# Performance work log

Measured on AMD Instinct MI355X. Metric: run time of the kernel, lower is better.

## Reference

```python
import jax, jax.numpy as jnp
import numpy as np

DIM = 256
NUM_HEADS = 4
WINDOW = 64
EPS = 1e-6


def setup_inputs() -> dict:
    key = jax.random.key(0)
    ks = jax.random.split(key, 12)
    d = DIM
    s = 0.02
    return {
        "x": jax.random.normal(ks[0], (4, 2049, d), dtype=jnp.float32),
        "norm1_w": jnp.ones((d,), jnp.float32),
        "in_proj_w": jax.random.normal(ks[1], (3 * d, d), jnp.float32) * s,
        "in_proj_b": jnp.zeros((3 * d,), jnp.float32),
        "out_proj_w": jax.random.normal(ks[2], (d, d), jnp.float32) * s,
        "out_proj_b": jnp.zeros((d,), jnp.float32),
        "norm2_w": jnp.ones((d,), jnp.float32),
        "w1": jax.random.normal(ks[3], (2 * d, d), jnp.float32) * s,
        "b1": jnp.zeros((2 * d,), jnp.float32),
        "w2": jax.random.normal(ks[4], (d, 2 * d), jnp.float32) * s,
        "b2": jnp.zeros((d,), jnp.float32),
    }


def _rmsnorm(x, w):
    r = jax.lax.rsqrt(jnp.mean(x * x, axis=-1, keepdims=True) + EPS)
    return x * r * w


def _factorized_mask(size):
    # global token 0 attends/attended everywhere; others banded within WINDOW
    idx = jnp.arange(size)
    band = jnp.abs(idx[:, None] - idx[None, :]) <= WINDOW
    allowed = band | (idx[:, None] == 0) | (idx[None, :] == 0)
    return jnp.where(allowed, 0.0, -jnp.inf).astype(jnp.float32)


def reference(x, norm1_w, in_proj_w, in_proj_b, out_proj_w, out_proj_b,
              norm2_w, w1, b1, w2, b2):
    B, S, D = x.shape
    H = NUM_HEADS
    dh = D // H
    residual = x
    h = _rmsnorm(x, norm1_w)
    # fused qkv projection (torch MHA in_proj): [B,S,3D]
    qkv = h @ in_proj_w.T + in_proj_b
    q, k, v = jnp.split(qkv, 3, axis=-1)
    q = q.reshape(B, S, H, dh).transpose(0, 2, 1, 3)  # [B,H,S,dh]
    k = k.reshape(B, S, H, dh).transpose(0, 2, 1, 3)
    v = v.reshape(B, S, H, dh).transpose(0, 2, 1, 3)
    scores = jnp.einsum("bhqd,bhkd->bhqk", q, k) / jnp.sqrt(jnp.float32(dh))
    scores = scores + _factorized_mask(S)  # additive -inf mask
    attn = jax.nn.softmax(scores, axis=-1)
    ctx = jnp.einsum("bhqk,bhkd->bhqd", attn, v)
    ctx = ctx.transpose(0, 2, 1, 3).reshape(B, S, D)
    attn_out = ctx @ out_proj_w.T + out_proj_b
    x1 = residual + attn_out
    h2 = _rmsnorm(x1, norm2_w)
    ffn = jax.nn.gelu(h2 @ w1.T + b1, approximate=False) @ w2.T + b2
    return x1 + ffn
```

## Files before the change

### kernel.cpp

```cpp
#include <hip/hip_runtime.h>
#include <hip/hip_bf16.h>
#include <math.h>

#define BATCH 4
#define SEQ 2049
#define WIN 64
#define M_ROWS 8196
#define M_PAD 8320

#define QT16 129
#define NKB 10
#define PSTR 168
#define CSTR 264
#define VGUARD 64
#define VW 2256
#define QKSTR 512
#define NSPLIT 33
#define VT_F4 288768
#define KCS 520

typedef __attribute__((ext_vector_type(8))) short short8;
typedef __attribute__((ext_vector_type(4))) float f32x4;
typedef __hip_bfloat16 bf16;

__device__ __forceinline__ float b2f(short u) {
    union { unsigned int i; float f; } c;
    c.i = ((unsigned int)(unsigned short)u) << 16;
    return c.f;
}
__device__ __forceinline__ short f2b(float f) {
    bf16 h = __float2bfloat16(f);
    return *reinterpret_cast<short*>(&h);
}

__global__ __launch_bounds__(256) void prep_kernel(
        const float* __restrict__ wq, const float* __restrict__ wo,
        const float* __restrict__ w1, const float* __restrict__ w2,
        bf16* __restrict__ oq, bf16* __restrict__ oo,
        bf16* __restrict__ o1, bf16* __restrict__ o2,
        short* __restrict__ vT) {
    const int bi = blockIdx.x, tid = threadIdx.x;
    if (bi < 2048) {
        int i = bi * 256 + tid;
        if (i < 196608)      oq[i]          = __float2bfloat16(wq[i]);
        else if (i < 262144) oo[i - 196608] = __float2bfloat16(wo[i - 196608]);
        else if (i < 393216) o1[i - 262144] = __float2bfloat16(w1[i - 262144]);
        else                 o2[i - 393216] = __float2bfloat16(w2[i - 393216]);
        return;
    }
    int rowid = (bi - 2048) * 2 + (tid >> 7);
    short* vr = vT + (size_t)rowid * VW;
    int t = tid & 127;
    if (t < 64) vr[t] = 0;
    else {
        int u = t - 64;
        if (u < 143) vr[VGUARD + SEQ + u] = 0;
        if (u + 143 < 143) {}
    }
}

__global__ __launch_bounds__(256) void gemm_qkv(
        const float* __restrict__ x, const float* __restrict__ n1w,
        const bf16* __restrict__ B, const float* __restrict__ bias,
        bf16* __restrict__ qk, short* __restrict__ vT) {
    __shared__ __align__(16) short hA[32 * KCS];
    __shared__ __align__(16) short lB[8 * 128 * 8];
    const int tid = threadIdx.x, lane = tid & 63, wid = tid >> 6;
    const int m0 = blockIdx.x * 64;
    const int n0 = blockIdx.y * 128;
    const int wr = wid >> 1, wc = wid & 1;
    const int r = lane & 15, g = lane >> 4;

    {
        const float4 wv = reinterpret_cast<const float4*>(n1w)[lane];
        #pragma unroll
        for (int t = 0; t < 16; t++) {
            int rr = wid * 16 + t;
            int row = m0 + rr;
            int rowc = row < M_ROWS ? row : M_ROWS - 1;
            const float4 v = reinterpret_cast<const float4*>(x + (size_t)rowc * 256)[lane];
            float ss = v.x * v.x + v.y * v.y + v.z * v.z + v.w * v.w;
            #pragma unroll
            for (int o = 1; o < 64; o <<= 1) ss += __shfl_xor(ss, o, 64);
            float rs = rsqrtf(ss * (1.0f / 256.0f) + 1e-6f);
            short4 y;
            y.x = f2b(v.x * rs * wv.x);
            y.y = f2b(v.y * rs * wv.y);
            y.z = f2b(v.z * rs * wv.z);
            y.w = f2b(v.w * rs * wv.w);
            *reinterpret_cast<short4*>(&hA[(lane >> 1) * KCS + rr * 8 + (lane & 1) * 4]) = y;
        }
    }
    __syncthreads();

    f32x4 acc[2][4];
    #pragma unroll
    for (int i = 0; i < 2; i++)
        #pragma unroll
        for (int j = 0; j < 4; j++) acc[i][j] = (f32x4){0.f, 0.f, 0.f, 0.f};

    for (int k0 = 0; k0 < 256; k0 += 64) {
        const int kcb = k0 >> 3;
        #pragma unroll
        for (int it = 0; it < 4; ++it) {
            int c = it * 256 + tid;
            int kc = c >> 7, row = c & 127;
            __builtin_amdgcn_global_load_lds(
                (const __attribute__((address_space(1))) void*)(B + (size_t)(n0 + row) * 256 + k0 + kc * 8),
                (__attribute__((address_space(3))) void*)&lB[c * 8], 16, 0, 0);
        }
        __syncthreads();
        #pragma unroll
        for (int kk = 0; kk < 2; kk++) {
            short8 a[2], b[4];
            #pragma unroll
            for (int mi = 0; mi < 2; mi++)
                a[mi] = *reinterpret_cast<const short8*>(
                    &hA[(kcb + kk * 4 + g) * KCS + (wr * 32 + mi * 16 + r) * 8]);
            #pragma unroll
            for (int ni = 0; ni < 4; ni++)
                b[ni] = *reinterpret_cast<const short8*>(&lB[((kk * 4 + g) * 128 + wc * 64 + ni * 16 + r) * 8]);
            #pragma unroll
            for (int mi = 0; mi < 2; mi++)
                #pragma unroll
                for (int ni = 0; ni < 4; ni++)
                    acc[mi][ni] = __builtin_amdgcn_mfma_f32_16x16x32_bf16(a[mi], b[ni], acc[mi][ni], 0, 0, 0);
        }
        __syncthreads();
    }

    const int c0 = lane & 15, r0 = (lane >> 4) * 4;
    const bool isV = (n0 >= 512);
    #pragma unroll
    for (int mi = 0; mi < 2; mi++) {
        #pragma unroll
        for (int ni = 0; ni < 4; ni++) {
            int col = n0 + wc * 64 + ni * 16 + c0;
            float bv = bias[col];
            #pragma unroll
            for (int j = 0; j < 4; j++) {
                int row = m0 + wr * 32 + mi * 16 + r0 + j;
                if (row < M_ROWS) {
                    float v = acc[mi][ni][j] + bv;
                    if (!isV) {
                        qk[(size_t)row * QKSTR + col] = __float2bfloat16(v);
                    } else {
                        int dcol = col - 512, hh = dcol >> 6, d = dcol & 63;
                        int bb = row >> 11;
                        int js = row - bb * SEQ;
                        if (js < 0) { bb--; js += SEQ; }
                        vT[((size_t)((bb * 4 + hh) * 64 + d)) * VW + VGUARD + js] = f2b(v);
                    }
                }
            }
        }
    }
}

template<int MODE, int BM, int BN>
__global__ __launch_bounds__(256) void gemm_lds_k(
        const bf16* __restrict__ A, const bf16* __restrict__ B,
        const float* __restrict__ bias, const float* __restrict__ resid,
        void* __restrict__ C, int M, int N, int K) {
    constexpr int FM = BM / 32, FN = BN / 32;
    __shared__ __align__(16) short lA[8 * BM * 8];
    __shared__ __align__(16) short lB[8 * BN * 8];
    const int tid = threadIdx.x, lane = tid & 63, wid = tid >> 6;
    const int m0 = blockIdx.x * BM;
    const int n0 = blockIdx.y * BN;
    const int wr = wid >> 1, wc = wid & 1;
    const int r = lane & 15, g = lane >> 4;

    f32x4 acc[FM][FN];
    #pragma unroll
    for (int i = 0; i < FM; i++)
        #pragma unroll
        for (int j = 0; j < FN; j++) acc[i][j] = (f32x4){0.f, 0.f, 0.f, 0.f};

    for (int k0 = 0; k0 < K; k0 += 64) {
        #pragma unroll
        for (int it = 0; it < BM / 32; ++it) {
            int c = it * 256 + tid;
            int kc = c / BM, row = c % BM;
            __builtin_amdgcn_global_load_lds(
                (const __attribute__((address_space(1))) void*)(A + (size_t)(m0 + row) * K + k0 + kc * 8),
                (__attribute__((address_space(3))) void*)&lA[c * 8], 16, 0, 0);
        }
        #pragma unroll
        for (int it = 0; it < BN / 32; ++it) {
            int c = it * 256 + tid;
            int kc = c / BN, row = c % BN;
            __builtin_amdgcn_global_load_lds(
                (const __attribute__((address_space(1))) void*)(B + (size_t)(n0 + row) * K + k0 + kc * 8),
                (__attribute__((address_space(3))) void*)&lB[c * 8], 16, 0, 0);
        }
        __syncthreads();
        #pragma unroll
        for (int kk = 0; kk < 2; kk++) {
            short8 a[FM], b[FN];
            #pragma unroll
            for (int mi = 0; mi < FM; mi++)
                a[mi] = *reinterpret_cast<const short8*>(&lA[((kk * 4 + g) * BM + wr * (BM / 2) + mi * 16 + r) * 8]);
            #pragma unroll
            for (int ni = 0; ni < FN; ni++)
                b[ni] = *reinterpret_cast<const short8*>(&lB[((kk * 4 + g) * BN + wc * (BN / 2) + ni * 16 + r) * 8]);
            #pragma unroll
            for (int mi = 0; mi < FM; mi++)
                #pragma unroll
                for (int ni = 0; ni < FN; ni++)
                    acc[mi][ni] = __builtin_amdgcn_mfma_f32_16x16x32_bf16(a[mi], b[ni], acc[mi][ni], 0, 0, 0);
        }
        __syncthreads();
    }

    const int c0 = lane & 15, r0 = (lane >> 4) * 4;
    #pragma unroll
    for (int mi = 0; mi < FM; mi++) {
        #pragma unroll
        for (int ni = 0; ni < FN; ni++) {
            int col = n0 + wc * (BN / 2) + ni * 16 + c0;
            float bv = bias[col];
            #pragma unroll
            for (int j = 0; j < 4; j++) {
                int row = m0 + wr * (BM / 2) + mi * 16 + r0 + j;
                if (row < M) {
                    float v = acc[mi][ni][j] + bv;
                    if (MODE == 2) v = 0.5f * v * (1.0f + erff(v * 0.70710678118654752f));
                    if (MODE == 1) {
                        v += resid[(size_t)row * N + col];
                        reinterpret_cast<float*>(C)[(size_t)row * N + col] = v;
                    } else {
                        reinterpret_cast<bf16*>(C)[(size_t)row * N + col] = __float2bfloat16(v);
                    }
                }
            }
        }
    }
}

__global__ __launch_bounds__(256) void attn_partial_k(const bf16* __restrict__ qkb,
                                                      const short* __restrict__ vT,
                                                      float* __restrict__ part) {
    __shared__ float q_s[64];
    __shared__ float p_s[64];
    __shared__ float meta[2];
    __shared__ float osum[4][64];
    const short* qks = (const short*)qkb;
    const int tid = threadIdx.x;
    const int lane = tid & 63, wid = tid >> 6;
    const int bh = blockIdx.x / NSPLIT, s = blockIdx.x % NSPLIT;
    const int b = bh >> 2, h = bh & 3;
    const size_t base = (size_t)b * SEQ;
    const int j0 = s * 64;
    if (tid < 64) q_s[tid] = b2f(qks[base * QKSTR + h * 64 + tid]);
    __syncthreads();
    if (wid == 0) {
        int j = j0 + lane;
        float sc = -1e30f;
        if (j < SEQ) {
            const short8* kp = reinterpret_cast<const short8*>(qks + (base + j) * QKSTR + 256 + h * 64);
            float acc = 0.f;
            #pragma unroll
            for (int d8 = 0; d8 < 8; ++d8) {
                short8 kv = kp[d8];
                #pragma unroll
                for (int e = 0; e < 8; ++e) acc += q_s[d8 * 8 + e] * b2f(kv[e]);
            }
            sc = acc * 0.125f;
        }
        float mx = sc;
        #pragma unroll
        for (int o = 1; o < 64; o <<= 1) mx = fmaxf(mx, __shfl_xor(mx, o, 64));
        float pv = (j < SEQ) ? expf(sc - mx) : 0.f;
        p_s[lane] = pv;
        float l = pv;
        #pragma unroll
        for (int o = 1; o < 64; o <<= 1) l += __shfl_xor(l, o, 64);
        if (lane == 0) { meta[0] = mx; meta[1] = l; }
    }
    __syncthreads();
    const short* vrow = vT + ((size_t)bh * 64 + lane) * VW + VGUARD + j0;
    float oa = 0.f;
    #pragma unroll
    for (int i0 = 0; i0 < 16; i0++) {
        int i = wid + i0 * 4;
        if (j0 + i < SEQ) oa += p_s[i] * b2f(vrow[i]);
    }
    osum[wid][lane] = oa;
    __syncthreads();
    if (wid == 0) {
        float o = osum[0][lane] + osum[1][lane] + osum[2][lane] + osum[3][lane];
        float* pp = part + (size_t)blockIdx.x * 66;
        pp[lane] = o;
        if (lane == 0) { pp[64] = meta[0]; pp[65] = meta[1]; }
    }
}

__global__ __launch_bounds__(256) void attn_or_k(
        const bf16* __restrict__ qkb, const short* __restrict__ vT,
        const float* __restrict__ part, const bf16* __restrict__ wo,
        const float* __restrict__ ob, const float* __restrict__ x,
        const float* __restrict__ nw, float* __restrict__ x1, bf16* __restrict__ h2) {
    __shared__ short pl[4 * 16 * PSTR];
    __shared__ short cl[16 * CSTR];
    __shared__ float osq[4][16];
    const short* qks = (const short*)qkb;
    const int tid = threadIdx.x, lane = tid & 63, h = tid >> 6;
    const int qt = blockIdx.x % QT16;
    const int b = blockIdx.x / QT16;
    const int bh = b * 4 + h;
    const size_t rbase = (size_t)b * SEQ;
    const int q0 = qt * 16;
    const int jbase = q0 - 64;
    const int lrow = lane & 15;
    const int koff = (lane >> 4) * 8;
    const int c0 = lrow, r0 = (lane >> 4) * 4;

    int qrow = q0 + lrow; if (qrow > SEQ - 1) qrow = SEQ - 1;
    const short* qp = qks + (rbase + qrow) * QKSTR + h * 64;
    short8 aq0 = *reinterpret_cast<const short8*>(qp + koff);
    short8 aq1 = *reinterpret_cast<const short8*>(qp + 32 + koff);

    const short* k0p = qks + rbase * QKSTR + 256 + h * 64;
    short8 k0a = *reinterpret_cast<const short8*>(k0p + koff);
    short8 k0b = *reinterpret_cast<const short8*>(k0p + 32 + koff);
    float s0 = 0.f;
    #pragma unroll
    for (int e = 0; e < 8; e++)
        s0 += b2f(aq0[e]) * b2f(k0a[e]) + b2f(aq1[e]) * b2f(k0b[e]);
    s0 += __shfl_xor(s0, 16, 64);
    s0 += __shfl_xor(s0, 32, 64);

    f32x4 s[NKB];
    #pragma unroll
    for (int n = 0; n < NKB; n++) {
        int j = jbase + n * 16 + lrow;
        int jc = j < 0 ? 0 : (j > SEQ - 1 ? SEQ - 1 : j);
        const short* kp = qks + (rbase + jc) * QKSTR + 256 + h * 64;
        short8 bk0 = *reinterpret_cast<const short8*>(kp + koff);
        short8 bk1 = *reinterpret_cast<const short8*>(kp + 32 + koff);
        f32x4 acc = (f32x4){0.f, 0.f, 0.f, 0.f};
        acc = __builtin_amdgcn_mfma_f32_16x16x32_bf16(aq0, bk0, acc, 0, 0, 0);
        acc = __builtin_amdgcn_mfma_f32_16x16x32_bf16(aq1, bk1, acc, 0, 0, 0);
        s[n] = acc;
    }

    const float SC = 0.125f * 1.44269504088896340736f;
    const bool g1 = (jbase > 0);
    float s0q[4], m4[4];
    #pragma unroll
    for (int jj = 0; jj < 4; jj++) {
        s0q[jj] = __shfl(s0, r0 + jj, 64) * SC;
        m4[jj] = g1 ? s0q[jj] : -1e30f;
    }
    #pragma unroll
    for (int n = 0; n < NKB; n++) {
        int j = jbase + n * 16 + c0;
        bool jv = (j >= 0) && (j < SEQ);
        #pragma unroll
        for (int jj = 0; jj < 4; jj++) {
            int q = q0 + r0 + jj;
            int dd = q - j; if (dd < 0) dd = -dd;
            bool allowed = jv && (dd <= WIN || j == 0);
            float v = allowed ? s[n][jj] * SC : -1e30f;
            s[n][jj] = v;
            m4[jj] = fmaxf(m4[jj], v);
        }
    }
    #pragma unroll
    for (int o = 1; o < 16; o <<= 1) {
        #pragma unroll
        for (int jj = 0; jj < 4; jj++) m4[jj] = fmaxf(m4[jj], __shfl_xor(m4[jj], o, 64));
    }

    float p0[4], l4[4];
    #pragma unroll
    for (int jj = 0; jj < 4; jj++) {
        p0[jj] = g1 ? exp2f(s0q[jj] - m4[jj]) : 0.f;
        l4[jj] = p0[jj];
    }
    #pragma unroll
    for (int n = 0; n < NKB; n++) {
        #pragma unroll
        for (int jj = 0; jj < 4; jj++) {
            float pv = exp2f(s[n][jj] - m4[jj]);
            l4[jj] += pv;
            pl[(h * 16 + r0 + jj) * PSTR + n * 16 + c0] = f2b(pv);
        }
    }
    #pragma unroll
    for (int o = 1; o < 16; o <<= 1) {
        #pragma unroll
        for (int jj = 0; jj < 4; jj++) l4[jj] += __shfl_xor(l4[jj], o, 64);
    }

    f32x4 o4[4];
    #pragma unroll
    for (int dn = 0; dn < 4; dn++) o4[dn] = (f32x4){0.f, 0.f, 0.f, 0.f};
    #pragma unroll
    for (int ks = 0; ks < NKB / 2; ks++) {
        short8 ap = *reinterpret_cast<const short8*>(&pl[(h * 16 + lrow) * PSTR + ks * 32 + koff]);
        int cc = VGUARD + jbase + ks * 32 + koff;
        #pragma unroll
        for (int dn = 0; dn < 4; dn++) {
            short8 bv = *reinterpret_cast<const short8*>(
                vT + ((size_t)bh * 64 + dn * 16 + lrow) * VW + cc);
            o4[dn] = __builtin_amdgcn_mfma_f32_16x16x32_bf16(ap, bv, o4[dn], 0, 0, 0);
        }
    }

    #pragma unroll
    for (int jj = 0; jj < 4; jj++) {
        int q = q0 + r0 + jj;
        int ql = r0 + jj;
        float rl = 1.0f / l4[jj];
        #pragma unroll
        for (int dn = 0; dn < 4; dn++) {
            float v0 = b2f(vT[((size_t)bh * 64 + dn * 16 + c0) * VW + VGUARD]);
            float val = (o4[dn][jj] + p0[jj] * v0) * rl;
            if (q >= 1) cl[ql * CSTR + h * 64 + dn * 16 + c0] = f2b(val);
        }
    }

    if (qt == 0) {
        float m = (lane < NSPLIT) ? part[(size_t)(bh * NSPLIT + lane) * 66 + 64] : -1e30f;
        #pragma unroll
        for (int o2 = 1; o2 < 64; o2 <<= 1) m = fmaxf(m, __shfl_xor(m, o2, 64));
        float L = 0.f, ov = 0.f;
        for (int sp = 0; sp < NSPLIT; sp++) {
            const float* pp = part + (size_t)(bh * NSPLIT + sp) * 66;
            float w = expf(pp[64] - m);
            L += pp[65] * w;
            ov += pp[lane] * w;
        }
        cl[0 * CSTR + h * 64 + lane] = f2b(ov / L);
    }
    __syncthreads();

    f32x4 oacc[4];
    #pragma unroll
    for (int ni = 0; ni < 4; ni++) oacc[ni] = (f32x4){0.f, 0.f, 0.f, 0.f};
    #pragma unroll
    for (int ks = 0; ks < 8; ks++) {
        short8 a = *reinterpret_cast<const short8*>(&cl[lrow * CSTR + ks * 32 + koff]);
        #pragma unroll
        for (int ni = 0; ni < 4; ni++) {
            short8 bfrag = *reinterpret_cast<const short8*>(
                reinterpret_cast<const short*>(wo) + (size_t)(h * 64 + ni * 16 + lrow) * 256 + ks * 32 + koff);
            oacc[ni] = __builtin_amdgcn_mfma_f32_16x16x32_bf16(a, bfrag, oacc[ni], 0, 0, 0);
        }
    }

    float ssq[4];
    #pragma unroll
    for (int jj = 0; jj < 4; jj++) {
        int row = q0 + r0 + jj;
        float sq = 0.f;
        if (row < SEQ) {
            #pragma unroll
            for (int ni = 0; ni < 4; ni++) {
                int col = h * 64 + ni * 16 + c0;
                float v = oacc[ni][jj] + ob[col] + x[(rbase + row) * 256 + col];
                oacc[ni][jj] = v;
                x1[(rbase + row) * 256 + col] = v;
                sq += v * v;
            }
        }
        ssq[jj] = sq;
    }
    #pragma unroll
    for (int o2 = 1; o2 < 16; o2 <<= 1) {
        #pragma unroll
        for (int jj = 0; jj < 4; jj++) ssq[jj] += __shfl_xor(ssq[jj], o2, 64);
    }
    if (c0 == 0) {
        #pragma unroll
        for (int jj = 0; jj < 4; jj++) osq[h][r0 + jj] = ssq[jj];
    }
    __syncthreads();
    #pragma unroll
    for (int jj = 0; jj < 4; jj++) {
        int lr = r0 + jj;
        int row = q0 + lr;
        if (row < SEQ) {
            float tot = osq[0][lr] + osq[1][lr] + osq[2][lr] + osq[3][lr];
            float rs = rsqrtf(tot * (1.0f / 256.0f) + 1e-6f);
            #pragma unroll
            for (int ni = 0; ni < 4; ni++) {
                int col = h * 64 + ni * 16 + c0;
                h2[(rbase + row) * 256 + col] = __float2bfloat16(oacc[ni][jj] * rs * nw[col]);
            }
        }
    }
}

extern "C" void kernel_launch(void* const* d_in, const int* in_sizes, int n_in,
                              void* d_out, int out_size, void* d_ws, size_t ws_size,
                              hipStream_t stream) {
    const float* x         = (const float*)d_in[0];
    const float* norm1_w   = (const float*)d_in[1];
    const float* in_proj_w = (const float*)d_in[2];
    const float* in_proj_b = (const float*)d_in[3];
    const float* out_proj_w= (const float*)d_in[4];
    const float* out_proj_b= (const float*)d_in[5];
    const float* norm2_w   = (const float*)d_in[6];
    const float* w1        = (const float*)d_in[7];
    const float* b1        = (const float*)d_in[8];
    const float* w2        = (const float*)d_in[9];
    const float* b2        = (const float*)d_in[10];
    float* out = (float*)d_out;

    char* ws = (char*)d_ws;
    size_t off = 0;
    auto take = [&](size_t bytes) {
        char* q = ws + off;
        off = (off + bytes + 255) & ~(size_t)255;
        return q;
    };
    bf16* qk_bf  = (bf16*)take((size_t)M_PAD * QKSTR * 2);
    float* x1    = (float*)take((size_t)M_PAD * 256 * 4);
    bf16* h2_bf  = (bf16*)take((size_t)M_PAD * 256 * 2);
    bf16* g_bf   = (bf16*)take((size_t)M_PAD * 512 * 2);
    bf16* wq_bf  = (bf16*)take(768 * 256 * 2);
    bf16* wo_bf  = (bf16*)take(256 * 256 * 2);
    bf16* w1_bf  = (bf16*)take(512 * 256 * 2);
    bf16* w2_bf  = (bf16*)take(256 * 512 * 2);
    float* part  = (float*)take((size_t)16 * NSPLIT * 66 * 4);
    short* vT    = (short*)take((size_t)16 * 64 * VW * 2);
    (void)ws_size; (void)in_sizes; (void)n_in; (void)out_size;

    prep_kernel<<<dim3(2560), dim3(256), 0, stream>>>(
        in_proj_w, out_proj_w, w1, w2, wq_bf, wo_bf, w1_bf, w2_bf, vT);
    gemm_qkv<<<dim3(130, 6), dim3(256), 0, stream>>>(x, norm1_w, wq_bf, in_proj_b, qk_bf, vT);
    attn_partial_k<<<dim3(16 * NSPLIT), dim3(256), 0, stream>>>(qk_bf, vT, part);
    attn_or_k<<<dim3(4 * QT16), dim3(256), 0, stream>>>(
        qk_bf, vT, part, wo_bf, out_proj_b, x, norm2_w, x1, h2_bf);
    gemm_lds_k<2, 64, 128><<<dim3(130, 4), dim3(256), 0, stream>>>(
        h2_bf, w1_bf, b1, (const float*)nullptr, (void*)g_bf, M_ROWS, 512, 256);
    gemm_lds_k<1, 64, 64><<<dim3(130, 4), dim3(256), 0, stream>>>(
        g_bf, w2_bf, b2, x1, (void*)out, M_ROWS, 256, 512);
}
```

Measured before the change: 118.0 us.

## Hoist RMSNorm out of QKV GEMM and overlap weight casts with attention

The first RMSNorm moves out of the QKV GEMM prologue into prep_kernel. It is computed once per row into a bf16 buffer instead of once per column block, which removed six fp32 reads of x per row. The QKV GEMM now streams the A tile into LDS with global_load_lds, like B. The out-proj and FFN weight conversions move into extra blocks of the attention partial kernel so they run alongside attention work. The cost is an extra bf16 activation round-trip through memory and a larger workspace.

```diff
diff --git a/kernel.cpp b/kernel.cpp
--- a/kernel.cpp
+++ b/kernel.cpp
@@ -16,8 +16,6 @@
 #define VW 2256
 #define QKSTR 512
 #define NSPLIT 33
-#define VT_F4 288768
-#define KCS 520
 
 typedef __attribute__((ext_vector_type(8))) short short8;
 typedef __attribute__((ext_vector_type(4))) float f32x4;
@@ -34,64 +32,50 @@
 }
 
 __global__ __launch_bounds__(256) void prep_kernel(
-        const float* __restrict__ wq, const float* __restrict__ wo,
-        const float* __restrict__ w1, const float* __restrict__ w2,
-        bf16* __restrict__ oq, bf16* __restrict__ oo,
-        bf16* __restrict__ o1, bf16* __restrict__ o2,
-        short* __restrict__ vT) {
+        const float* __restrict__ wq, bf16* __restrict__ oq,
+        const float* __restrict__ x, const float* __restrict__ nw,
+        bf16* __restrict__ h, short* __restrict__ vT) {
     const int bi = blockIdx.x, tid = threadIdx.x;
-    if (bi < 2048) {
+    if (bi < 768) {
         int i = bi * 256 + tid;
-        if (i < 196608)      oq[i]          = __float2bfloat16(wq[i]);
-        else if (i < 262144) oo[i - 196608] = __float2bfloat16(wo[i - 196608]);
-        else if (i < 393216) o1[i - 262144] = __float2bfloat16(w1[i - 262144]);
-        else                 o2[i - 393216] = __float2bfloat16(w2[i - 393216]);
+        oq[i] = __float2bfloat16(wq[i]);
         return;
     }
-    int rowid = (bi - 2048) * 2 + (tid >> 7);
-    short* vr = vT + (size_t)rowid * VW;
-    int t = tid & 127;
-    if (t < 64) vr[t] = 0;
-    else {
-        int u = t - 64;
-        if (u < 143) vr[VGUARD + SEQ + u] = 0;
-        if (u + 143 < 143) {}
-    }
+    if (bi >= 2817) {
+        int rowid = (bi - 2817) * 2 + (tid >> 7);
+        short* vr = vT + (size_t)rowid * VW;
+        int t = tid & 127;
+        if (t < 64) vr[t] = 0;
+        else if (t - 64 < 143) vr[VGUARD + SEQ + (t - 64)] = 0;
+        return;
+    }
+    int wid = tid >> 6, lane = tid & 63;
+    int row = (bi - 768) * 4 + wid;
+    if (row >= M_ROWS) return;
+    const float4 v = reinterpret_cast<const float4*>(x + (size_t)row * 256)[lane];
+    float ss = v.x * v.x + v.y * v.y + v.z * v.z + v.w * v.w;
+    #pragma unroll
+    for (int o = 1; o < 64; o <<= 1) ss += __shfl_xor(ss, o, 64);
+    float r = rsqrtf(ss * (1.0f / 256.0f) + 1e-6f);
+    const float4 wv = reinterpret_cast<const float4*>(nw)[lane];
+    bf16* hp = h + (size_t)row * 256 + lane * 4;
+    hp[0] = __float2bfloat16(v.x * r * wv.x);
+    hp[1] = __float2bfloat16(v.y * r * wv.y);
+    hp[2] = __float2bfloat16(v.z * r * wv.z);
+    hp[3] = __float2bfloat16(v.w * r * wv.w);
 }
 
 __global__ __launch_bounds__(256) void gemm_qkv(
-        const float* __restrict__ x, const float* __restrict__ n1w,
-        const bf16* __restrict__ B, const float* __restrict__ bias,
-        bf16* __restrict__ qk, short* __restrict__ vT) {
-    __shared__ __align__(16) short hA[32 * KCS];
+        const bf16* __restrict__ A, const bf16* __restrict__ B,
+        const float* __restrict__ bias, bf16* __restrict__ qk, short* __restrict__ vT) {
+    __shared__ __align__(16) short lA[8 * 64 * 8];
     __shared__ __align__(16) short lB[8 * 128 * 8];
     const int tid = threadIdx.x, lane = tid & 63, wid = tid >> 6;
     const int m0 = blockIdx.x * 64;
     const int n0 = blockIdx.y * 128;
     const int wr = wid >> 1, wc = wid & 1;
     const int r = lane & 15, g = lane >> 4;
-
-    {
-        const float4 wv = reinterpret_cast<const float4*>(n1w)[lane];
-        #pragma unroll
-        for (int t = 0; t < 16; t++) {
-            int rr = wid * 16 + t;
-            int row = m0 + rr;
-            int rowc = row < M_ROWS ? row : M_ROWS - 1;
-            const float4 v = reinterpret_cast<const float4*>(x + (size_t)rowc * 256)[lane];
-            float ss = v.x * v.x + v.y * v.y + v.z * v.z + v.w * v.w;
-            #pragma unroll
-            for (int o = 1; o < 64; o <<= 1) ss += __shfl_xor(ss, o, 64);
-            float rs = rsqrtf(ss * (1.0f / 256.0f) + 1e-6f);
-            short4 y;
-            y.x = f2b(v.x * rs * wv.x);
-            y.y = f2b(v.y * rs * wv.y);
-            y.z = f2b(v.z * rs * wv.z);
-            y.w = f2b(v.w * rs * wv.w);
-            *reinterpret_cast<short4*>(&hA[(lane >> 1) * KCS + rr * 8 + (lane & 1) * 4]) = y;
-        }
-    }
-    __syncthreads();
+    const int K = 256;
 
     f32x4 acc[2][4];
     #pragma unroll
@@ -99,14 +83,21 @@
         #pragma unroll
         for (int j = 0; j < 4; j++) acc[i][j] = (f32x4){0.f, 0.f, 0.f, 0.f};
 
-    for (int k0 = 0; k0 < 256; k0 += 64) {
-        const int kcb = k0 >> 3;
+    for (int k0 = 0; k0 < K; k0 += 64) {
+        #pragma unroll
+        for (int it = 0; it < 2; ++it) {
+            int c = it * 256 + tid;
+            int kc = c >> 6, row = c & 63;
+            __builtin_amdgcn_global_load_lds(
+                (const __attribute__((address_space(1))) void*)(A + (size_t)(m0 + row) * K + k0 + kc * 8),
+                (__attribute__((address_space(3))) void*)&lA[c * 8], 16, 0, 0);
+        }
         #pragma unroll
         for (int it = 0; it < 4; ++it) {
             int c = it * 256 + tid;
             int kc = c >> 7, row = c & 127;
             __builtin_amdgcn_global_load_lds(
-                (const __attribute__((address_space(1))) void*)(B + (size_t)(n0 + row) * 256 + k0 + kc * 8),
+                (const __attribute__((address_space(1))) void*)(B + (size_t)(n0 + row) * K + k0 + kc * 8),
                 (__attribute__((address_space(3))) void*)&lB[c * 8], 16, 0, 0);
         }
         __syncthreads();
@@ -115,8 +106,7 @@
             short8 a[2], b[4];
             #pragma unroll
             for (int mi = 0; mi < 2; mi++)
-                a[mi] = *reinterpret_cast<const short8*>(
-                    &hA[(kcb + kk * 4 + g) * KCS + (wr * 32 + mi * 16 + r) * 8]);
+                a[mi] = *reinterpret_cast<const short8*>(&lA[((kk * 4 + g) * 64 + wr * 32 + mi * 16 + r) * 8]);
             #pragma unroll
             for (int ni = 0; ni < 4; ni++)
                 b[ni] = *reinterpret_cast<const short8*>(&lB[((kk * 4 + g) * 128 + wc * 64 + ni * 16 + r) * 8]);
@@ -239,14 +229,23 @@
 }
 
 __global__ __launch_bounds__(256) void attn_partial_k(const bf16* __restrict__ qkb,
-                                                      const short* __restrict__ vT,
-                                                      float* __restrict__ part) {
+        const short* __restrict__ vT, float* __restrict__ part,
+        const float* __restrict__ wo_f, const float* __restrict__ w1_f,
+        const float* __restrict__ w2_f, bf16* __restrict__ wob,
+        bf16* __restrict__ w1b, bf16* __restrict__ w2b) {
+    const int tid = threadIdx.x;
+    if (blockIdx.x >= 528) {
+        int i = (blockIdx.x - 528) * 256 + tid;
+        if (i < 65536)       wob[i]          = __float2bfloat16(wo_f[i]);
+        else if (i < 196608) w1b[i - 65536]  = __float2bfloat16(w1_f[i - 65536]);
+        else                 w2b[i - 196608] = __float2bfloat16(w2_f[i - 196608]);
+        return;
+    }
     __shared__ float q_s[64];
     __shared__ float p_s[64];
     __shared__ float meta[2];
     __shared__ float osum[4][64];
     const short* qks = (const short*)qkb;
-    const int tid = threadIdx.x;
     const int lane = tid & 63, wid = tid >> 6;
     const int bh = blockIdx.x / NSPLIT, s = blockIdx.x % NSPLIT;
     const int b = bh >> 2, h = bh & 3;
@@ -517,6 +516,7 @@
         off = (off + bytes + 255) & ~(size_t)255;
         return q;
     };
+    bf16* h_bf   = (bf16*)take((size_t)M_PAD * 256 * 2);
     bf16* qk_bf  = (bf16*)take((size_t)M_PAD * QKSTR * 2);
     float* x1    = (float*)take((size_t)M_PAD * 256 * 4);
     bf16* h2_bf  = (bf16*)take((size_t)M_PAD * 256 * 2);
@@ -529,10 +529,11 @@
     short* vT    = (short*)take((size_t)16 * 64 * VW * 2);
     (void)ws_size; (void)in_sizes; (void)n_in; (void)out_size;
 
-    prep_kernel<<<dim3(2560), dim3(256), 0, stream>>>(
-        in_proj_w, out_proj_w, w1, w2, wq_bf, wo_bf, w1_bf, w2_bf, vT);
-    gemm_qkv<<<dim3(130, 6), dim3(256), 0, stream>>>(x, norm1_w, wq_bf, in_proj_b, qk_bf, vT);
-    attn_partial_k<<<dim3(16 * NSPLIT), dim3(256), 0, stream>>>(qk_bf, vT, part);
+    prep_kernel<<<dim3(3329), dim3(256), 0, stream>>>(
+        in_proj_w, wq_bf, x, norm1_w, h_bf, vT);
+    gemm_qkv<<<dim3(130, 6), dim3(256), 0, stream>>>(h_bf, wq_bf, in_proj_b, qk_bf, vT);
+    attn_partial_k<<<dim3(1808), dim3(256), 0, stream>>>(
+        qk_bf, vT, part, out_proj_w, w1, w2, wo_bf, w1_bf, w2_bf);
     attn_or_k<<<dim3(4 * QT16), dim3(256), 0, stream>>>(
         qk_bf, vT, part, wo_bf, out_proj_b, x, norm2_w, x1, h2_bf);
     gemm_lds_k<2, 64, 128><<<dim3(130, 4), dim3(256), 0, stream>>>(
```

After: 114.0 us (median of 3 runs). 3.5% less time.
